# Performance work log

Hardware: AMD Instinct MI355X
Metric: run time of the kernel (lower is better)

## Reference

```python
import jax, jax.numpy as jnp
import numpy as np

S, N, CM, CZ, H, D = 512, 768, 64, 128, 8, 32
EPS = 1e-5


def _layer_norm(x, w, b):
    mu = jnp.mean(x, axis=-1, keepdims=True)
    xc = x - mu
    var = jnp.mean(xc * xc, axis=-1, keepdims=True)
    return xc * jax.lax.rsqrt(var + EPS) * w + b


def setup_inputs() -> dict:
    key = jax.random.key(0)
    ks = jax.random.split(key, 6)
    scale_m = 1.0 / np.sqrt(CM)
    scale_z = 1.0 / np.sqrt(CZ)
    scale_o = 1.0 / np.sqrt(H * D)
    return {
        "m": jax.random.normal(ks[0], (1, S, N, CM), jnp.float32),
        "z": jax.random.normal(ks[1], (1, N, N, CZ), jnp.float32),
        "norm_m_w": jnp.ones((CM,), jnp.float32),
        "norm_m_b": jnp.zeros((CM,), jnp.float32),
        "norm_z_w": jnp.ones((CZ,), jnp.float32),
        "norm_z_b": jnp.zeros((CZ,), jnp.float32),
        "wm": jax.random.normal(ks[2], (CM, H * D), jnp.float32) * scale_m,
        "wg": jax.random.normal(ks[3], (CM, H * D), jnp.float32) * scale_m,
        "wz": jax.random.normal(ks[4], (CZ, H), jnp.float32) * scale_z,
        "wo": jax.random.normal(ks[5], (H * D, CM), jnp.float32) * scale_o,
    }


def reference(m, z, norm_m_w, norm_m_b, norm_z_w, norm_z_b, wm, wg, wz, wo):
    m0 = m[0]  # [S, N, CM]
    z0 = z[0]  # [N, N, CZ]
    mn = _layer_norm(m0, norm_m_w, norm_m_b)
    zn = _layer_norm(z0, norm_z_w, norm_z_b)
    # b[p,q,h]; original code softmaxes over the LAST axis of b'[h,p,q] (axis q)
    # but contracts as o[s,q] = sum_p w[p,q] v[s,p] (transpose_a matmul),
    # so softmax is over axis q = axis 1 of [p,q,h].
    b = jnp.einsum('pqc,ch->pqh', zn, wz)
    w = jax.nn.softmax(b, axis=1)  # normalized over q for each p (faithful to source)
    v = jnp.einsum('spc,ck->spk', mn, wm).reshape(S, N, H, D)
    g = jax.nn.sigmoid(jnp.einsum('spc,ck->spk', mn, wg)).reshape(S, N, H, D)
    o = jnp.einsum('pqh,sphd->sqhd', w, v) * g  # weighted average then gate
    out = jnp.einsum('sqhd,hdc->sqc', o, wo.reshape(H, D, CM))
    return out[None]  # [1, S, N, CM]
```

## Files before the change

### kernel.cpp

```cpp
#include <hip/hip_runtime.h>
#include <hip/hip_bf16.h>
#include <stdint.h>

#define S_DIM 512
#define N_DIM 768
#define CMd   64
#define CZd   128
#define Hd    8
#define Dd    32
#define HDd   256

typedef float          f32x4  __attribute__((ext_vector_type(4)));
typedef __bf16         bf16x8 __attribute__((ext_vector_type(8)));
typedef unsigned int   u32x4  __attribute__((ext_vector_type(4)));
typedef unsigned int   u32x2  __attribute__((ext_vector_type(2)));
typedef unsigned short u16x8  __attribute__((ext_vector_type(8)));

__device__ __forceinline__ unsigned short f2bf(float f) {
  __bf16 h = (__bf16)f;
  return __builtin_bit_cast(unsigned short, h);
}
__device__ __forceinline__ float bf2f(unsigned short u) {
  unsigned int x = ((unsigned int)u) << 16;
  return __builtin_bit_cast(float, x);
}
__device__ __forceinline__ float sigmoidf_(float x) {
  return 1.f / (1.f + __expf(-x));
}

typedef __attribute__((address_space(1))) const void cg_void;
typedef __attribute__((address_space(3))) void lds_void;
__device__ __forceinline__ void async16(const unsigned short* g, unsigned short* l) {
  __builtin_amdgcn_global_load_lds((cg_void*)g, (lds_void*)l, 16, 0, 0);
}

__global__ __launch_bounds__(256) void k0_prep(const float* __restrict__ wm,
                                               const float* __restrict__ wg,
                                               const float* __restrict__ wo,
                                               unsigned short* __restrict__ WBT,
                                               unsigned short* __restrict__ woT) {
  int t = blockIdx.x * 256 + threadIdx.x;
  if (t < 512 * 64) {
    int j = t >> 6, c = t & 63;
    float v = (j < 256) ? wm[c * 256 + j] : wg[c * 256 + (j - 256)];
    WBT[t] = f2bf(v);
  }
  if (t < 64 * 256) {
    int c = t >> 8, k = t & 255;
    woT[t] = f2bf(wo[k * 64 + c]);
  }
}

__global__ __launch_bounds__(256) void k1_zln_b(const float* __restrict__ z,
                                                const float* __restrict__ nzw,
                                                const float* __restrict__ nzb,
                                                const float* __restrict__ wz,
                                                float* __restrict__ b_e) {
  __shared__ float wzT[8][128];
  int t = threadIdx.x;
  for (int i = t; i < 1024; i += 256) {
    int h = i >> 7, c = i & 127;
    wzT[h][c] = wz[c * 8 + h];
  }
  __syncthreads();

  int lane = t & 63, w = t >> 6;
  int sub = lane & 7;
  int rloc = lane >> 3;
  int p = blockIdx.y;
  int q = blockIdx.x * 32 + w * 8 + rloc;

  const float* zr = z + ((size_t)p * N_DIM + q) * CZd + sub * 16;
  f32x4 v[4];
#pragma unroll
  for (int j = 0; j < 4; j++) v[j] = *(const f32x4*)(zr + 4 * j);

  float s1 = 0.f, s2 = 0.f;
#pragma unroll
  for (int j = 0; j < 4; j++)
#pragma unroll
    for (int e = 0; e < 4; e++) { float x = v[j][e]; s1 += x; s2 += x * x; }
  s1 += __shfl_xor(s1, 1); s2 += __shfl_xor(s2, 1);
  s1 += __shfl_xor(s1, 2); s2 += __shfl_xor(s2, 2);
  s1 += __shfl_xor(s1, 4); s2 += __shfl_xor(s2, 4);
  float mean = s1 * (1.f / 128.f);
  float var  = s2 * (1.f / 128.f) - mean * mean;
  float rstd = rsqrtf(var + 1e-5f);

  const float* wp = nzw + sub * 16;
  const float* bp = nzb + sub * 16;
  float zn[16];
#pragma unroll
  for (int j = 0; j < 4; j++) {
    f32x4 wv = *(const f32x4*)(wp + 4 * j);
    f32x4 bv = *(const f32x4*)(bp + 4 * j);
#pragma unroll
    for (int e = 0; e < 4; e++)
      zn[j * 4 + e] = (v[j][e] - mean) * rstd * wv[e] + bv[e];
  }

  float accb[8];
#pragma unroll
  for (int h = 0; h < 8; h++) {
    const f32x4* wr = (const f32x4*)&wzT[h][sub * 16];
    float a = 0.f;
#pragma unroll
    for (int j = 0; j < 4; j++) {
      f32x4 ww = wr[j];
#pragma unroll
      for (int e = 0; e < 4; e++) a += zn[j * 4 + e] * ww[e];
    }
    accb[h] = a;
  }
#pragma unroll
  for (int mask = 1; mask <= 4; mask <<= 1)
#pragma unroll
    for (int h = 0; h < 8; h++) accb[h] += __shfl_xor(accb[h], mask);

  float outv = accb[0];
#pragma unroll
  for (int h = 1; h < 8; h++) outv = (sub == h) ? accb[h] : outv;
  b_e[((size_t)p * 8 + sub) * 768 + q] = outv;
}

__global__ __launch_bounds__(256) void k1b_softmax(float* __restrict__ b_e,
                                                   float* __restrict__ invs) {
  int row = blockIdx.x;
  int t = threadIdx.x;
  float* base = b_e + (size_t)row * 768;
  float x0 = base[t], x1 = base[t + 256], x2 = base[t + 512];
  __shared__ float red[256];
  red[t] = fmaxf(x0, fmaxf(x1, x2));
  __syncthreads();
  for (int o = 128; o > 0; o >>= 1) {
    if (t < o) red[t] = fmaxf(red[t], red[t + o]);
    __syncthreads();
  }
  float M = red[0];
  __syncthreads();
  float e0 = __expf(x0 - M), e1 = __expf(x1 - M), e2 = __expf(x2 - M);
  base[t] = e0; base[t + 256] = e1; base[t + 512] = e2;
  red[t] = e0 + e1 + e2;
  __syncthreads();
  for (int o = 128; o > 0; o >>= 1) {
    if (t < o) red[t] += red[t + o];
    __syncthreads();
  }
  if (t == 0) invs[row] = 1.0f / red[0];
}

__global__ __launch_bounds__(256) void k1b2_transpose(const float* __restrict__ b_e,
                                                      const float* __restrict__ invs,
                                                      unsigned short* __restrict__ Aw) {
  int t = threadIdx.x;
  int q0 = blockIdx.x * 64, p0 = blockIdx.y * 64, h = blockIdx.z;
  __shared__ unsigned short T[64][65];
  int i = t >> 2, ch = t & 3;
  size_t rowid = (size_t)(p0 + i) * 8 + h;
  const float* src = b_e + rowid * 768 + q0 + ch * 16;
  float inv = invs[rowid];
#pragma unroll
  for (int jj = 0; jj < 16; jj += 4) {
    f32x4 v = *(const f32x4*)(src + jj);
#pragma unroll
    for (int e = 0; e < 4; e++) T[i][ch * 16 + jj + e] = f2bf(v[e] * inv);
  }
  __syncthreads();
  int j = i;
  unsigned short outv[16];
#pragma unroll
  for (int ii = 0; ii < 16; ii++) outv[ii] = T[ch * 16 + ii][j];
  int rx = (j & 7) << 3;
  unsigned short* dstrow = Aw + ((size_t)h * 768 + q0 + j) * 768 + p0;
  *(u32x4*)(dstrow + ((ch * 16) ^ rx))     = *(u32x4*)(outv);
  *(u32x4*)(dstrow + ((ch * 16 + 8) ^ rx)) = *(u32x4*)(outv + 8);
}

__global__ __launch_bounds__(256) void k2_mln_vg(const float* __restrict__ mp,
                                                 const float* __restrict__ nmw,
                                                 const float* __restrict__ nmb,
                                                 const unsigned short* __restrict__ WBT,
                                                 unsigned short* __restrict__ VT,
                                                 unsigned short* __restrict__ G) {
  __shared__ unsigned short WBs[512 * 64];
  __shared__ unsigned short As[64 * 64];
  int t = threadIdx.x;
  int p0 = blockIdx.x * 64, s = blockIdx.y;

#pragma unroll
  for (int it = 0; it < 16; it++) {
    int cid = t + it * 256;
    int row = cid >> 3, ch = cid & 7;
    u32x4 v = *(const u32x4*)(WBT + row * 64 + ch * 8);
    *(u32x4*)(WBs + row * 64 + ((ch * 8) ^ ((row & 7) << 3))) = v;
  }

  {
    int row = t >> 2, qt = t & 3;
    const float* mr = mp + ((size_t)s * N_DIM + p0 + row) * CMd + qt * 16;
    f32x4 v[4];
#pragma unroll
    for (int j = 0; j < 4; j++) v[j] = *(const f32x4*)(mr + 4 * j);
    float s1 = 0.f, s2 = 0.f;
#pragma unroll
    for (int j = 0; j < 4; j++)
#pragma unroll
      for (int e = 0; e < 4; e++) { float x = v[j][e]; s1 += x; s2 += x * x; }
    s1 += __shfl_xor(s1, 1); s2 += __shfl_xor(s2, 1);
    s1 += __shfl_xor(s1, 2); s2 += __shfl_xor(s2, 2);
    float mean = s1 * (1.f / 64.f);
    float var  = s2 * (1.f / 64.f) - mean * mean;
    float rstd = rsqrtf(var + 1e-5f);
    unsigned short o[16];
#pragma unroll
    for (int j = 0; j < 4; j++) {
      f32x4 wv = *(const f32x4*)(nmw + qt * 16 + 4 * j);
      f32x4 bv = *(const f32x4*)(nmb + qt * 16 + 4 * j);
#pragma unroll
      for (int e = 0; e < 4; e++)
        o[j * 4 + e] = f2bf((v[j][e] - mean) * rstd * wv[e] + bv[e]);
    }
    int k0 = qt * 16;
    *(u32x4*)(As + row * 64 + ((k0) ^ ((row & 7) << 3)))     = *(u32x4*)(o);
    *(u32x4*)(As + row * 64 + ((k0 + 8) ^ ((row & 7) << 3))) = *(u32x4*)(o + 8);
  }
  __syncthreads();

  int lane = t & 63, w = t >> 6;
  int n0 = w * 128;
  int lr = lane & 15, lk8 = (lane >> 4) * 8;
  f32x4 zero = {0.f, 0.f, 0.f, 0.f};
  f32x4 acc[4][8];
#pragma unroll
  for (int i = 0; i < 4; i++)
#pragma unroll
    for (int j = 0; j < 8; j++) acc[i][j] = zero;

#pragma unroll
  for (int kk = 0; kk < 2; kk++) {
    bf16x8 bfr[8];
#pragma unroll
    for (int nt = 0; nt < 8; nt++) {
      int r = n0 + nt * 16 + lr;
      bfr[nt] = *(const bf16x8*)(WBs + r * 64 + ((kk * 32 + lk8) ^ ((r & 7) << 3)));
    }
#pragma unroll
    for (int mt = 0; mt < 4; mt++) {
      int ar = mt * 16 + lr;
      bf16x8 a = *(const bf16x8*)(As + ar * 64 + ((kk * 32 + lk8) ^ ((ar & 7) << 3)));
#pragma unroll
      for (int nt = 0; nt < 8; nt++)
        acc[mt][nt] = __builtin_amdgcn_mfma_f32_16x16x32_bf16(a, bfr[nt], acc[mt][nt], 0, 0, 0);
    }
  }

#pragma unroll
  for (int mt = 0; mt < 4; mt++)
#pragma unroll
    for (int nt = 0; nt < 8; nt++) {
      int j = n0 + nt * 16 + lr;
      int ploc = mt * 16 + (lane >> 4) * 4;
      if (j < 256) {
        int h = j >> 5, d = j & 31;
        unsigned short pk[4];
#pragma unroll
        for (int r = 0; r < 4; r++) pk[r] = f2bf(acc[mt][nt][r]);
        int pswz = ((((ploc >> 3) ^ (lr & 7)) << 3) | (ploc & 7));
        *(u32x2*)(VT + ((size_t)h * 16384 + s * 32 + d) * 768 + p0 + pswz) = *(u32x2*)pk;
      } else {
        int jj = j - 256;
#pragma unroll
        for (int r = 0; r < 4; r++)
          G[((size_t)s * 768 + p0 + ploc + r) * 256 + jj] = f2bf(sigmoidf_(acc[mt][nt][r]));
      }
    }
}

__global__ __launch_bounds__(256) void k3_gemm(const unsigned short* __restrict__ Aw,
                                               const unsigned short* __restrict__ VT,
                                               unsigned short* __restrict__ O) {
  __shared__ unsigned short Asl[128 * 64];
  __shared__ unsigned short Bsl[128 * 64];
  int t = threadIdx.x;
  int flat = blockIdx.x;
  int h = blockIdx.y;
  int f2 = (flat & 7) * 96 + (flat >> 3);
  int mt_b = f2 % 6, nt_b = f2 / 6;
  int q0 = mt_b * 128, n0 = nt_b * 128;

  const unsigned short* Ab = Aw + (size_t)h * 768 * 768 + (size_t)q0 * 768;
  const unsigned short* Bb = VT + (size_t)h * 16384 * 768 + (size_t)n0 * 768;

  int lane = t & 63, w = t >> 6;
  int wr = (w >> 1) * 64, wc = (w & 1) * 64;
  int lr = lane & 15;

  const unsigned short* gA = Ab + (size_t)(w * 32 + (lane >> 3)) * 768 + (lane & 7) * 8;
  const unsigned short* gB = Bb + (size_t)(w * 32 + (lane >> 3)) * 768 + (lane & 7) * 8;
  unsigned short* lA = Asl + w * 2048;
  unsigned short* lB = Bsl + w * 2048;

  f32x4 zero = {0.f, 0.f, 0.f, 0.f};
  f32x4 acc[4][4];
#pragma unroll
  for (int i = 0; i < 4; i++)
#pragma unroll
    for (int j = 0; j < 4; j++) acc[i][j] = zero;

  for (int kt = 0; kt < 12; kt++) {
    int ko = kt * 64;
#pragma unroll
    for (int i = 0; i < 4; i++) {
      async16(gA + (size_t)i * 8 * 768 + ko, lA + i * 512);
      async16(gB + (size_t)i * 8 * 768 + ko, lB + i * 512);
    }
    asm volatile("s_waitcnt vmcnt(0)" ::: "memory");
    __builtin_amdgcn_sched_barrier(0);
    __syncthreads();
#pragma unroll
    for (int kk = 0; kk < 2; kk++) {
      int kc = kk * 32 + (lane >> 4) * 8;
      bf16x8 afr[4], bfr[4];
#pragma unroll
      for (int i = 0; i < 4; i++) {
        int arr = wr + i * 16 + lr;
        int brr = wc + i * 16 + lr;
        afr[i] = *(const bf16x8*)(Asl + arr * 64 + (kc ^ ((arr & 7) << 3)));
        bfr[i] = *(const bf16x8*)(Bsl + brr * 64 + (kc ^ ((brr & 7) << 3)));
      }
#pragma unroll
      for (int mt = 0; mt < 4; mt++)
#pragma unroll
        for (int nt = 0; nt < 4; nt++)
          acc[mt][nt] = __builtin_amdgcn_mfma_f32_16x16x32_bf16(afr[mt], bfr[nt], acc[mt][nt], 0, 0, 0);
    }
    __syncthreads();
  }

#pragma unroll
  for (int mt = 0; mt < 4; mt++)
#pragma unroll
    for (int nt = 0; nt < 4; nt++) {
      int q = q0 + wr + mt * 16 + (lane >> 4) * 4;
      int n = n0 + wc + nt * 16 + lr;
      int s_ = n >> 5, d = n & 31;
      size_t ob = ((size_t)s_ * 768 + q) * 256 + h * 32 + d;
#pragma unroll
      for (int r = 0; r < 4; r++)
        O[ob + (size_t)r * 256] = f2bf(acc[mt][nt][r]);
    }
}

__global__ __launch_bounds__(256) void k4_out(const unsigned short* __restrict__ O,
                                              const unsigned short* __restrict__ G,
                                              const unsigned short* __restrict__ woT,
                                              float* __restrict__ out) {
  __shared__ unsigned short OGs[64 * 256];
  __shared__ unsigned short WOs[64 * 256];
  int t = threadIdx.x;
  int q0 = blockIdx.x * 64, s = blockIdx.y;

#pragma unroll
  for (int it = 0; it < 8; it++) {
    int cid = t + it * 256;
    int row = cid >> 5, ch = cid & 31;
    u32x4 v = *(const u32x4*)(woT + row * 256 + ch * 8);
    *(u32x4*)(WOs + row * 256 + ((ch * 8) ^ ((row & 7) << 3))) = v;
  }

  int i = t >> 2, c4 = t & 3;
  const unsigned short* Orow = O + ((size_t)s * 768 + q0 + i) * 256 + c4 * 64;
  const unsigned short* Grow = G + ((size_t)s * 768 + q0 + i) * 256 + c4 * 64;
#pragma unroll
  for (int jj = 0; jj < 8; jj++) {
    u16x8 ov = *(const u16x8*)(Orow + jj * 8);
    u16x8 gv = *(const u16x8*)(Grow + jj * 8);
    unsigned short pk[8];
#pragma unroll
    for (int e = 0; e < 8; e++) pk[e] = f2bf(bf2f(ov[e]) * bf2f(gv[e]));
    *(u32x4*)(OGs + i * 256 + ((c4 * 64 + jj * 8) ^ ((i & 7) << 3))) = *(u32x4*)pk;
  }
  __syncthreads();

  int lane = t & 63, w = t >> 6;
  int lr = lane & 15, lk8 = (lane >> 4) * 8;
  f32x4 zero = {0.f, 0.f, 0.f, 0.f};
  f32x4 acc[4];
#pragma unroll
  for (int nt = 0; nt < 4; nt++) acc[nt] = zero;

#pragma unroll
  for (int kk = 0; kk < 8; kk++) {
    int ar = w * 16 + lr;
    bf16x8 a = *(const bf16x8*)(OGs + ar * 256 + ((kk * 32 + lk8) ^ ((ar & 7) << 3)));
#pragma unroll
    for (int nt = 0; nt < 4; nt++) {
      int br = nt * 16 + lr;
      bf16x8 b = *(const bf16x8*)(WOs + br * 256 + ((kk * 32 + lk8) ^ ((br & 7) << 3)));
      acc[nt] = __builtin_amdgcn_mfma_f32_16x16x32_bf16(a, b, acc[nt], 0, 0, 0);
    }
  }

#pragma unroll
  for (int nt = 0; nt < 4; nt++) {
    int q = q0 + w * 16 + (lane >> 4) * 4;
    int c = nt * 16 + lr;
    float* dst = out + ((size_t)s * 768 + q) * 64 + c;
#pragma unroll
    for (int r = 0; r < 4; r++) dst[(size_t)r * 64] = acc[nt][r];
  }
}

extern "C" void kernel_launch(void* const* d_in, const int* in_sizes, int n_in,
                              void* d_out, int out_size, void* d_ws, size_t ws_size,
                              hipStream_t stream) {
  const float* m   = (const float*)d_in[0];
  const float* z   = (const float*)d_in[1];
  const float* nmw = (const float*)d_in[2];
  const float* nmb = (const float*)d_in[3];
  const float* nzw = (const float*)d_in[4];
  const float* nzb = (const float*)d_in[5];
  const float* wm  = (const float*)d_in[6];
  const float* wg  = (const float*)d_in[7];
  const float* wz  = (const float*)d_in[8];
  const float* wo  = (const float*)d_in[9];
  float* out = (float*)d_out;

  char* ws = (char*)d_ws;
  size_t off = 0;
  auto alloc = [&](size_t bytes) -> void* {
    void* p = ws + off;
    off += (bytes + 1023) & ~(size_t)1023;
    return p;
  };
  float*          b_e  = (float*)alloc((size_t)768 * 8 * 768 * 4);
  float*          invs = (float*)alloc((size_t)768 * 8 * 4);
  unsigned short* Awt  = (unsigned short*)alloc((size_t)8 * 768 * 768 * 2);
  unsigned short* WBT  = (unsigned short*)alloc((size_t)512 * 64 * 2);
  unsigned short* woT  = (unsigned short*)alloc((size_t)64 * 256 * 2);
  unsigned short* VT   = (unsigned short*)alloc((size_t)8 * 16384 * 768 * 2);
  unsigned short* G    = (unsigned short*)alloc((size_t)512 * 768 * 256 * 2);
  unsigned short* O    = (unsigned short*)alloc((size_t)512 * 768 * 256 * 2);
  if (ws_size < off) return;

  k0_prep<<<128, 256, 0, stream>>>(wm, wg, wo, WBT, woT);
  k1_zln_b<<<dim3(24, 768), 256, 0, stream>>>(z, nzw, nzb, wz, b_e);
  k1b_softmax<<<6144, 256, 0, stream>>>(b_e, invs);
  k1b2_transpose<<<dim3(12, 12, 8), 256, 0, stream>>>(b_e, invs, Awt);
  k2_mln_vg<<<dim3(12, 512), 256, 0, stream>>>(m, nmw, nmb, WBT, VT, G);
  k3_gemm<<<dim3(768, 8), 256, 0, stream>>>(Awt, VT, O);
  k4_out<<<dim3(12, 512), 256, 0, stream>>>(O, G, woT, out);
}
```

Baseline: 694.6 us.

## Fuse head-wise attention GEMM with gating and output projection across heads

Merges the per-head weighted-average GEMM and the gated output-projection kernel into one kernel. Each block loops over all 8 heads, applies the sigmoid gate in registers, stages the gated tile in shared memory and accumulates the output projection in registers. This removes the full bf16 intermediate O tensor, which was written once and read back once. It also adds double-buffered async loads. In exchange the N tile shrinks from 128 to 64, so the softmax-weight matrix is re-read more often. The gate values are now read with scattered 2-byte loads and the wo weights directly from global memory.

```diff
diff --git a/kernel.cpp b/kernel.cpp
--- a/kernel.cpp
+++ b/kernel.cpp
@@ -276,139 +276,134 @@
     }
 }
 
-__global__ __launch_bounds__(256) void k3_gemm(const unsigned short* __restrict__ Aw,
-                                               const unsigned short* __restrict__ VT,
-                                               unsigned short* __restrict__ O) {
-  __shared__ unsigned short Asl[128 * 64];
-  __shared__ unsigned short Bsl[128 * 64];
+__global__ __launch_bounds__(256) void k34_fused(const unsigned short* __restrict__ Aw,
+                                                 const unsigned short* __restrict__ VT,
+                                                 const unsigned short* __restrict__ G,
+                                                 const unsigned short* __restrict__ woT,
+                                                 float* __restrict__ out) {
+  __shared__ unsigned short Asl[2][128 * 64];
+  __shared__ unsigned short Bsl[2][64 * 64];
   int t = threadIdx.x;
   int flat = blockIdx.x;
-  int h = blockIdx.y;
-  int f2 = (flat & 7) * 96 + (flat >> 3);
-  int mt_b = f2 % 6, nt_b = f2 / 6;
-  int q0 = mt_b * 128, n0 = nt_b * 128;
-
-  const unsigned short* Ab = Aw + (size_t)h * 768 * 768 + (size_t)q0 * 768;
-  const unsigned short* Bb = VT + (size_t)h * 16384 * 768 + (size_t)n0 * 768;
+  int xcd = flat & 7, idx = flat >> 3;
+  int n_idx = xcd * 32 + idx / 6;
+  int q_idx = idx % 6;
+  int q0 = q_idx * 128, n0 = n_idx * 64;
+  int s0 = n0 >> 5;
 
   int lane = t & 63, w = t >> 6;
-  int wr = (w >> 1) * 64, wc = (w & 1) * 64;
-  int lr = lane & 15;
-
-  const unsigned short* gA = Ab + (size_t)(w * 32 + (lane >> 3)) * 768 + (lane & 7) * 8;
-  const unsigned short* gB = Bb + (size_t)(w * 32 + (lane >> 3)) * 768 + (lane & 7) * 8;
-  unsigned short* lA = Asl + w * 2048;
-  unsigned short* lB = Bsl + w * 2048;
+  int wq = w >> 1, wn = w & 1;
+  int wr = wq * 64;
+  int wc = wn * 32;
+  int lr = lane & 15, lg = lane >> 4;
+
+  const size_t aOff = (size_t)(q0 + w * 32 + (lane >> 3)) * 768 + (lane & 7) * 8;
+  const size_t bOff = (size_t)(n0 + w * 16 + (lane >> 3)) * 768 + (lane & 7) * 8;
+
+  auto STAGE = [&](int h, int kt, int buf) {
+    const unsigned short* a = Aw + (size_t)h * 589824 + aOff + kt * 64;
+    const unsigned short* b = VT + (size_t)h * 12582912 + bOff + kt * 64;
+    unsigned short* la = &Asl[buf][w * 2048];
+    unsigned short* lb = &Bsl[buf][w * 1024];
+#pragma unroll
+    for (int i = 0; i < 4; i++) async16(a + (size_t)i * 6144, la + i * 512);
+#pragma unroll
+    for (int i = 0; i < 2; i++) async16(b + (size_t)i * 6144, lb + i * 512);
+  };
 
   f32x4 zero = {0.f, 0.f, 0.f, 0.f};
-  f32x4 acc[4][4];
-#pragma unroll
-  for (int i = 0; i < 4; i++)
-#pragma unroll
-    for (int j = 0; j < 4; j++) acc[i][j] = zero;
-
-  for (int kt = 0; kt < 12; kt++) {
-    int ko = kt * 64;
-#pragma unroll
-    for (int i = 0; i < 4; i++) {
-      async16(gA + (size_t)i * 8 * 768 + ko, lA + i * 512);
-      async16(gB + (size_t)i * 8 * 768 + ko, lB + i * 512);
-    }
-    asm volatile("s_waitcnt vmcnt(0)" ::: "memory");
+  f32x4 oh[4][2];
+  f32x4 oc[4][4];
+#pragma unroll
+  for (int i = 0; i < 4; i++) {
+#pragma unroll
+    for (int j = 0; j < 2; j++) oh[i][j] = zero;
+#pragma unroll
+    for (int j = 0; j < 4; j++) oc[i][j] = zero;
+  }
+
+  STAGE(0, 0, 0);
+  asm volatile("s_waitcnt vmcnt(0)" ::: "memory");
+  __builtin_amdgcn_sched_barrier(0);
+  __syncthreads();
+
+  for (int h = 0; h < 8; h++) {
+    for (int kt = 0; kt < 12; kt++) {
+      int cur = kt & 1;
+      if (kt < 11)      STAGE(h, kt + 1, cur ^ 1);
+      else if (h < 7)   STAGE(h + 1, 0, cur ^ 1);
+#pragma unroll
+      for (int kk = 0; kk < 2; kk++) {
+        int kc = kk * 32 + lg * 8;
+        bf16x8 af[4], bfv[2];
+#pragma unroll
+        for (int i = 0; i < 4; i++) {
+          int arr = wr + i * 16 + lr;
+          af[i] = *(const bf16x8*)(&Asl[cur][arr * 64 + (kc ^ ((arr & 7) << 3))]);
+        }
+#pragma unroll
+        for (int j = 0; j < 2; j++) {
+          int brr = wc + j * 16 + lr;
+          bfv[j] = *(const bf16x8*)(&Bsl[cur][brr * 64 + (kc ^ ((brr & 7) << 3))]);
+        }
+#pragma unroll
+        for (int mt = 0; mt < 4; mt++)
+#pragma unroll
+          for (int nt = 0; nt < 2; nt++)
+            oh[mt][nt] = __builtin_amdgcn_mfma_f32_16x16x32_bf16(af[mt], bfv[nt], oh[mt][nt], 0, 0, 0);
+      }
+      asm volatile("s_waitcnt vmcnt(0)" ::: "memory");
+      __builtin_amdgcn_sched_barrier(0);
+      __syncthreads();
+    }
+
+    unsigned short* slab = &Asl[1][w * 2048];
+    int sg = s0 + wn;
+#pragma unroll
+    for (int mt = 0; mt < 4; mt++)
+#pragma unroll
+      for (int nt = 0; nt < 2; nt++) {
+        int d = nt * 16 + lr;
+        int qg = q0 + wr + mt * 16 + lg * 4;
+        const unsigned short* gp = G + ((size_t)sg * 768 + qg) * 256 + h * 32 + d;
+#pragma unroll
+        for (int r = 0; r < 4; r++) {
+          float g = bf2f(gp[(size_t)r * 256]);
+          int ql = mt * 16 + lg * 4 + r;
+          slab[ql * 32 + (d ^ ((ql & 3) << 3))] = f2bf(oh[mt][nt][r] * g);
+          oh[mt][nt][r] = 0.f;
+        }
+      }
+    asm volatile("s_waitcnt lgkmcnt(0)" ::: "memory");
     __builtin_amdgcn_sched_barrier(0);
-    __syncthreads();
-#pragma unroll
-    for (int kk = 0; kk < 2; kk++) {
-      int kc = kk * 32 + (lane >> 4) * 8;
-      bf16x8 afr[4], bfr[4];
-#pragma unroll
-      for (int i = 0; i < 4; i++) {
-        int arr = wr + i * 16 + lr;
-        int brr = wc + i * 16 + lr;
-        afr[i] = *(const bf16x8*)(Asl + arr * 64 + (kc ^ ((arr & 7) << 3)));
-        bfr[i] = *(const bf16x8*)(Bsl + brr * 64 + (kc ^ ((brr & 7) << 3)));
-      }
-#pragma unroll
-      for (int mt = 0; mt < 4; mt++)
-#pragma unroll
-        for (int nt = 0; nt < 4; nt++)
-          acc[mt][nt] = __builtin_amdgcn_mfma_f32_16x16x32_bf16(afr[mt], bfr[nt], acc[mt][nt], 0, 0, 0);
-    }
-    __syncthreads();
-  }
-
-#pragma unroll
-  for (int mt = 0; mt < 4; mt++)
-#pragma unroll
-    for (int nt = 0; nt < 4; nt++) {
-      int q = q0 + wr + mt * 16 + (lane >> 4) * 4;
-      int n = n0 + wc + nt * 16 + lr;
-      int s_ = n >> 5, d = n & 31;
-      size_t ob = ((size_t)s_ * 768 + q) * 256 + h * 32 + d;
-#pragma unroll
-      for (int r = 0; r < 4; r++)
-        O[ob + (size_t)r * 256] = f2bf(acc[mt][nt][r]);
-    }
-}
-
-__global__ __launch_bounds__(256) void k4_out(const unsigned short* __restrict__ O,
-                                              const unsigned short* __restrict__ G,
-                                              const unsigned short* __restrict__ woT,
-                                              float* __restrict__ out) {
-  __shared__ unsigned short OGs[64 * 256];
-  __shared__ unsigned short WOs[64 * 256];
-  int t = threadIdx.x;
-  int q0 = blockIdx.x * 64, s = blockIdx.y;
-
-#pragma unroll
-  for (int it = 0; it < 8; it++) {
-    int cid = t + it * 256;
-    int row = cid >> 5, ch = cid & 31;
-    u32x4 v = *(const u32x4*)(woT + row * 256 + ch * 8);
-    *(u32x4*)(WOs + row * 256 + ((ch * 8) ^ ((row & 7) << 3))) = v;
-  }
-
-  int i = t >> 2, c4 = t & 3;
-  const unsigned short* Orow = O + ((size_t)s * 768 + q0 + i) * 256 + c4 * 64;
-  const unsigned short* Grow = G + ((size_t)s * 768 + q0 + i) * 256 + c4 * 64;
-#pragma unroll
-  for (int jj = 0; jj < 8; jj++) {
-    u16x8 ov = *(const u16x8*)(Orow + jj * 8);
-    u16x8 gv = *(const u16x8*)(Grow + jj * 8);
-    unsigned short pk[8];
-#pragma unroll
-    for (int e = 0; e < 8; e++) pk[e] = f2bf(bf2f(ov[e]) * bf2f(gv[e]));
-    *(u32x4*)(OGs + i * 256 + ((c4 * 64 + jj * 8) ^ ((i & 7) << 3))) = *(u32x4*)pk;
-  }
-  __syncthreads();
-
-  int lane = t & 63, w = t >> 6;
-  int lr = lane & 15, lk8 = (lane >> 4) * 8;
-  f32x4 zero = {0.f, 0.f, 0.f, 0.f};
-  f32x4 acc[4];
-#pragma unroll
-  for (int nt = 0; nt < 4; nt++) acc[nt] = zero;
-
-#pragma unroll
-  for (int kk = 0; kk < 8; kk++) {
-    int ar = w * 16 + lr;
-    bf16x8 a = *(const bf16x8*)(OGs + ar * 256 + ((kk * 32 + lk8) ^ ((ar & 7) << 3)));
-#pragma unroll
-    for (int nt = 0; nt < 4; nt++) {
-      int br = nt * 16 + lr;
-      bf16x8 b = *(const bf16x8*)(WOs + br * 256 + ((kk * 32 + lk8) ^ ((br & 7) << 3)));
-      acc[nt] = __builtin_amdgcn_mfma_f32_16x16x32_bf16(a, b, acc[nt], 0, 0, 0);
-    }
-  }
-
-#pragma unroll
-  for (int nt = 0; nt < 4; nt++) {
-    int q = q0 + w * 16 + (lane >> 4) * 4;
-    int c = nt * 16 + lr;
-    float* dst = out + ((size_t)s * 768 + q) * 64 + c;
-#pragma unroll
-    for (int r = 0; r < 4; r++) dst[(size_t)r * 64] = acc[nt][r];
-  }
+    bf16x8 pa[4];
+#pragma unroll
+    for (int mq = 0; mq < 4; mq++) {
+      int ql = mq * 16 + lr;
+      pa[mq] = *(const bf16x8*)(slab + ql * 32 + ((lg * 8) ^ ((ql & 3) << 3)));
+    }
+#pragma unroll
+    for (int nc = 0; nc < 4; nc++) {
+      bf16x8 wb = *(const bf16x8*)(woT + (size_t)(nc * 16 + lr) * 256 + h * 32 + lg * 8);
+#pragma unroll
+      for (int mq = 0; mq < 4; mq++)
+        oc[mq][nc] = __builtin_amdgcn_mfma_f32_16x16x32_bf16(pa[mq], wb, oc[mq][nc], 0, 0, 0);
+    }
+    asm volatile("s_waitcnt lgkmcnt(0)" ::: "memory");
+    __builtin_amdgcn_sched_barrier(0);
+  }
+
+  int sg = s0 + wn;
+#pragma unroll
+  for (int mq = 0; mq < 4; mq++)
+#pragma unroll
+    for (int nc = 0; nc < 4; nc++) {
+      int c = nc * 16 + lr;
+      int qg = q0 + wr + mq * 16 + lg * 4;
+      float* dst = out + ((size_t)sg * 768 + qg) * 64 + c;
+#pragma unroll
+      for (int r = 0; r < 4; r++) dst[(size_t)r * 64] = oc[mq][nc][r];
+    }
 }
 
 extern "C" void kernel_launch(void* const* d_in, const int* in_sizes, int n_in,
@@ -440,7 +435,6 @@
   unsigned short* woT  = (unsigned short*)alloc((size_t)64 * 256 * 2);
   unsigned short* VT   = (unsigned short*)alloc((size_t)8 * 16384 * 768 * 2);
   unsigned short* G    = (unsigned short*)alloc((size_t)512 * 768 * 256 * 2);
-  unsigned short* O    = (unsigned short*)alloc((size_t)512 * 768 * 256 * 2);
   if (ws_size < off) return;
 
   k0_prep<<<128, 256, 0, stream>>>(wm, wg, wo, WBT, woT);
@@ -448,6 +442,5 @@
   k1b_softmax<<<6144, 256, 0, stream>>>(b_e, invs);
   k1b2_transpose<<<dim3(12, 12, 8), 256, 0, stream>>>(b_e, invs, Awt);
   k2_mln_vg<<<dim3(12, 512), 256, 0, stream>>>(m, nmw, nmb, WBT, VT, G);
-  k3_gemm<<<dim3(768, 8), 256, 0, stream>>>(Awt, VT, O);
-  k4_out<<<dim3(12, 512), 256, 0, stream>>>(O, G, woT, out);
-}
+  k34_fused<<<dim3(1536), 256, 0, stream>>>(Awt, VT, G, woT, out);
+}
```

Result: slower. 757.7 us (+9.1%).
